# Performance work log

Measured on AMD Instinct MI355X. Metric: run time of the kernel, lower is better.

## Reference

```python
import jax, jax.numpy as jnp
import numpy as np
import math

VOCAB = 32000
HIDDEN = 256
N_HEADS = 8
HEAD_DIM = 32
MAX_LEN = 2048


def _pos_encoding(max_len, d_model, dtype=jnp.float32):
    # Matches PositionalEncoding buffer (even d_model).
    pos = jnp.arange(max_len, dtype=dtype)[:, None]                       # [L,1]
    div = jnp.exp(jnp.arange(0, d_model, 2, dtype=dtype) * (-(math.log(10000.0) / d_model)))
    ang = pos * div                                                        # [L, d/2]
    pe = jnp.zeros((max_len, d_model), dtype=dtype)
    pe = pe.at[:, 0::2].set(jnp.sin(ang))
    pe = pe.at[:, 1::2].set(jnp.cos(ang))
    return pe


def setup_inputs() -> dict:
    key = jax.random.key(0)
    ks = jax.random.split(key, 7)
    B, S = 8, 2047
    s = 0.02
    x = jax.random.randint(ks[0], (B, S), 0, VOCAB + 1, dtype=jnp.int64)
    emb_w = jax.random.normal(ks[1], (VOCAB + 1, HIDDEN), jnp.float32) * s
    wq = jax.random.normal(ks[2], (N_HEADS, HEAD_DIM, HIDDEN), jnp.float32) * s
    wk = jax.random.normal(ks[3], (N_HEADS, HEAD_DIM, HIDDEN), jnp.float32) * s
    wv = jax.random.normal(ks[4], (N_HEADS, HEAD_DIM, HIDDEN), jnp.float32) * s
    wo = jax.random.normal(ks[5], (HIDDEN, N_HEADS * HEAD_DIM), jnp.float32) * s
    wu = jax.random.normal(ks[6], (VOCAB + 1, HIDDEN), jnp.float32) * s
    return {"x": x, "emb_w": emb_w, "wq": wq, "wk": wk, "wv": wv, "wo": wo, "wu": wu}


def reference(x, emb_w, wq, wk, wv, wo, wu):
    B, S = x.shape
    # prepend CLS token (id=2)
    tok = jnp.concatenate([jnp.full((B, 1), 2, dtype=x.dtype), x], axis=1)  # [B, S+1]
    y = emb_w[tok]                                                          # [B, S+1, H]
    y = y + _pos_encoding(S + 1, HIDDEN, y.dtype)
    # batched per-head QKV (nn.Linear: out = in @ W.T)
    q = jnp.einsum('bsh,nkh->bnsk', y, wq)
    k = jnp.einsum('bsh,nkh->bnsk', y, wk)
    v = jnp.einsum('bsh,nkh->bnsk', y, wv)
    scores = jnp.einsum('bnsk,bntk->bnst', q, k) / (HEAD_DIM ** 0.5)        # [B,N,S+1,S+1]
    A = jax.nn.softmax(scores, axis=-1)
    o = jnp.einsum('bnst,bntk->bnsk', A, v)                                 # [B,N,S+1,K]
    o = jnp.transpose(o, (0, 2, 1, 3)).reshape(B, S + 1, N_HEADS * HEAD_DIM)
    att = o @ wo.T + y     # residual inside MultiHeadAttention
    y = att + y            # second residual in MultiHeadTransformerPosEmb.forward
    out = y[:, 0, :] @ wu.T                                                 # [B, VOCAB+1]
    return out
```

## Files before the change

kernel.cpp:

```cpp
#include <hip/hip_runtime.h>
#include <stdint.h>

#define B_   8
#define S_   2047
#define L_   2048
#define H_   256
#define NH_  8
#define HD_  32
#define V_   32001

__device__ __forceinline__ float foldx(float a, int off) {
    return a + __shfl_xor(a, off, 64);
}
__device__ __forceinline__ float sel8(const float a[8], int j) {
    float v = a[0];
    v = (j == 1) ? a[1] : v;
    v = (j == 2) ? a[2] : v;
    v = (j == 3) ? a[3] : v;
    v = (j == 4) ? a[4] : v;
    v = (j == 5) ? a[5] : v;
    v = (j == 6) ? a[6] : v;
    v = (j == 7) ? a[7] : v;
    return v;
}

__global__ __launch_bounds__(256) void k0_prep(const float* __restrict__ emb,
                                               const float* __restrict__ wq,
                                               const float* __restrict__ wk,
                                               float* __restrict__ qk,
                                               float* __restrict__ y0,
                                               int* __restrict__ counters) {
    __shared__ float y0_l[H_];
    __shared__ float q0p[HD_][8];
    __shared__ float q0_l[HD_];
    int n = blockIdx.x, tid = threadIdx.x;
    if (tid == 0) counters[n] = 0;
    float v = emb[2 * H_ + tid] + ((tid & 1) ? 1.0f : 0.0f);
    y0_l[tid] = v;
    if (n == 0) y0[tid] = v;
    __syncthreads();
    {
        int k = tid >> 3, part = tid & 7;
        const float* w = wq + (n * HD_ + k) * H_ + part * 32;
        const float* yy = y0_l + part * 32;
        float acc = 0.f;
#pragma unroll
        for (int j = 0; j < 32; ++j) acc += w[j] * yy[j];
        q0p[k][part] = acc;
    }
    __syncthreads();
    if (tid < HD_) {
        float s = 0.f;
#pragma unroll
        for (int j = 0; j < 8; ++j) s += q0p[tid][j];
        q0_l[tid] = s;
    }
    __syncthreads();
    float acc = 0.f;
    for (int k = 0; k < HD_; ++k)
        acc += q0_l[k] * wk[(n * HD_ + k) * H_ + tid];
    qk[n * H_ + tid] = acc * 0.17677669529663687f;
}

__global__ __launch_bounds__(256, 1) void k13_attn(const int* __restrict__ x,
                                                   const float* __restrict__ emb,
                                                   const float* __restrict__ qkw,
                                                   const float* __restrict__ wv,
                                                   const float* __restrict__ wo,
                                                   const float* __restrict__ y0g,
                                                   float* __restrict__ op_partial,
                                                   float* __restrict__ esum_blk,
                                                   float* __restrict__ z,
                                                   int* __restrict__ counters) {
    int bid = blockIdx.x;
    int b = bid >> 5, c = bid & 31;
    int tid = threadIdx.x, lane = tid & 63, w = tid >> 6;
    int t0 = c * 64 + w * 16;

    __shared__ float4 p_l4[64][2];
    __shared__ __align__(16) float red[4][NH_ * H_];
    __shared__ float es_l[4][NH_];
    __shared__ int is_last;
    __shared__ float inv_l[NH_];
    __shared__ float o_l[H_];

    float4 qr[NH_];
#pragma unroll
    for (int n = 0; n < NH_; ++n)
        qr[n] = *(const float4*)(qkw + n * H_ + lane * 4);

    const float cdiv = 0.07195578414202881f;
    float div0 = expf(-(float)(lane * 2) * cdiv);
    float div1 = expf(-(float)(lane * 2 + 1) * cdiv);
    float s0, c0, s1, c1, sd0, cd0, sd1, cd1;
    {
        float a0 = (float)t0 * div0, a1 = (float)t0 * div1;
        s0 = sinf(a0); c0 = cosf(a0); s1 = sinf(a1); c1 = cosf(a1);
        sd0 = sinf(div0); cd0 = cosf(div0);
        sd1 = sinf(div1); cd1 = cosf(div1);
    }

    float4 yreg[16];
    float es = 0.f;

#pragma unroll
    for (int i = 0; i < 16; ++i) {
        int t = t0 + i;
        int tok = (t == 0) ? 2 : x[b * S_ + t - 1];
        float4 ev = *(const float4*)(emb + (size_t)tok * H_ + lane * 4);
        float4 y4;
        y4.x = ev.x + s0; y4.y = ev.y + c0; y4.z = ev.z + s1; y4.w = ev.w + c1;
        yreg[i] = y4;
        float ns0 = s0 * cd0 + c0 * sd0; c0 = c0 * cd0 - s0 * sd0; s0 = ns0;
        float ns1 = s1 * cd1 + c1 * sd1; c1 = c1 * cd1 - s1 * sd1; s1 = ns1;

        float a[NH_];
#pragma unroll
        for (int n = 0; n < NH_; ++n)
            a[n] = qr[n].x * y4.x + qr[n].y * y4.y + qr[n].z * y4.z + qr[n].w * y4.w;
        float m4[4];
#pragma unroll
        for (int k = 0; k < 4; ++k) {
            float lo = foldx(a[k], 32), hi = foldx(a[k + 4], 32);
            m4[k] = (lane & 32) ? hi : lo;
        }
        float m2[2];
#pragma unroll
        for (int k = 0; k < 2; ++k) {
            float lo = foldx(m4[k], 16), hi = foldx(m4[k + 2], 16);
            m2[k] = (lane & 16) ? hi : lo;
        }
        float lo = foldx(m2[0], 8), hi = foldx(m2[1], 8);
        float m1 = (lane & 8) ? hi : lo;
        m1 = foldx(m1, 4); m1 = foldx(m1, 2); m1 = foldx(m1, 1);
        float e = __expf(m1);
        es += e;
        if ((lane & 7) == 0)
            ((float*)&p_l4[w * 16 + i][0])[lane >> 3] = e;
    }
    if ((lane & 7) == 0) es_l[w][lane >> 3] = es;

    float4 acc4[NH_];
#pragma unroll
    for (int n = 0; n < NH_; ++n) acc4[n] = make_float4(0.f, 0.f, 0.f, 0.f);
#pragma unroll
    for (int i = 0; i < 16; ++i) {
        float4 pA = p_l4[w * 16 + i][0];
        float4 pB = p_l4[w * 16 + i][1];
        float p[NH_] = {pA.x, pA.y, pA.z, pA.w, pB.x, pB.y, pB.z, pB.w};
        float4 y4 = yreg[i];
#pragma unroll
        for (int n = 0; n < NH_; ++n) {
            acc4[n].x += p[n] * y4.x;
            acc4[n].y += p[n] * y4.y;
            acc4[n].z += p[n] * y4.z;
            acc4[n].w += p[n] * y4.w;
        }
    }
#pragma unroll
    for (int n = 0; n < NH_; ++n)
        *(float4*)&red[w][n * H_ + lane * 4] = acc4[n];
    __syncthreads();
#pragma unroll
    for (int g = 0; g < 2; ++g) {
        int idx = tid * 8 + g * 4;
        float4 r0 = *(const float4*)&red[0][idx];
        float4 r1 = *(const float4*)&red[1][idx];
        float4 r2 = *(const float4*)&red[2][idx];
        float4 r3 = *(const float4*)&red[3][idx];
        float4 s;
        s.x = r0.x + r1.x + r2.x + r3.x;
        s.y = r0.y + r1.y + r2.y + r3.y;
        s.z = r0.z + r1.z + r2.z + r3.z;
        s.w = r0.w + r1.w + r2.w + r3.w;
        *(float4*)&red[0][idx] = s;
    }
    if (tid < NH_)
        esum_blk[bid * NH_ + tid] = es_l[0][tid] + es_l[1][tid] + es_l[2][tid] + es_l[3][tid];
    __syncthreads();
    {
        int n = tid >> 5;
        const float* wrow = wv + (size_t)tid * H_;
        const float* ps = &red[0][n * H_];
        float acc = 0.f;
#pragma unroll 16
        for (int h4 = 0; h4 < H_ / 4; ++h4) {
            float4 wv4 = *(const float4*)(wrow + h4 * 4);
            float4 p4 = *(const float4*)(ps + h4 * 4);
            acc += wv4.x * p4.x + wv4.y * p4.y + wv4.z * p4.z + wv4.w * p4.w;
        }
        op_partial[bid * H_ + tid] = acc;
    }

    __threadfence();
    __syncthreads();
    if (tid == 0) is_last = (atomicAdd(&counters[b], 1) == 31);
    __syncthreads();
    if (!is_last) return;
    __threadfence();

    if (tid < NH_) {
        float s = 0.f;
#pragma unroll
        for (int cc = 0; cc < 32; ++cc) s += esum_blk[(b * 32 + cc) * NH_ + tid];
        inv_l[tid] = 1.0f / s;
    }
    __syncthreads();
    {
        float s = 0.f;
#pragma unroll
        for (int cc = 0; cc < 32; ++cc) s += op_partial[(b * 32 + cc) * H_ + tid];
        o_l[tid] = s * inv_l[tid >> 5];
    }
    __syncthreads();
    {
        const float* wrow = wo + (size_t)tid * H_;
        float s = 0.f;
#pragma unroll 16
        for (int j4 = 0; j4 < H_ / 4; ++j4) {
            float4 w4 = *(const float4*)(wrow + j4 * 4);
            s += w4.x * o_l[j4 * 4] + w4.y * o_l[j4 * 4 + 1]
               + w4.z * o_l[j4 * 4 + 2] + w4.w * o_l[j4 * 4 + 3];
        }
        z[b * H_ + tid] = s + 2.0f * y0g[tid];
    }
}

__global__ __launch_bounds__(256) void k5_out(const float* __restrict__ z,
                                              const float* __restrict__ wu,
                                              float* __restrict__ out) {
    int tid = threadIdx.x, lane = tid & 63, w = tid >> 6;
    int m = lane & 15;
    int g = lane >> 4;
    int hb = m * 16;
    float zr[B_][16];
#pragma unroll
    for (int b = 0; b < B_; ++b)
#pragma unroll
        for (int jj = 0; jj < 4; ++jj)
            *(float4*)&zr[b][jj * 4] = *(const float4*)(z + b * H_ + hb + jj * 4);

    __shared__ float o_l[B_ * 65];
    int base = blockIdx.x * 64;
#pragma unroll
    for (int pass = 0; pass < 4; ++pass) {
        int rl = w * 16 + pass * 4 + g;
        int v = base + rl;
        int vc = (v < V_) ? v : (V_ - 1);
        const float* wr = wu + (size_t)vc * H_ + hb;
        float4 w0 = *(const float4*)(wr);
        float4 w1 = *(const float4*)(wr + 4);
        float4 w2 = *(const float4*)(wr + 8);
        float4 w3 = *(const float4*)(wr + 12);
        float acc[B_];
#pragma unroll
        for (int b = 0; b < B_; ++b) {
            acc[b] = zr[b][0] * w0.x + zr[b][1] * w0.y + zr[b][2] * w0.z + zr[b][3] * w0.w
                   + zr[b][4] * w1.x + zr[b][5] * w1.y + zr[b][6] * w1.z + zr[b][7] * w1.w
                   + zr[b][8] * w2.x + zr[b][9] * w2.y + zr[b][10] * w2.z + zr[b][11] * w2.w
                   + zr[b][12] * w3.x + zr[b][13] * w3.y + zr[b][14] * w3.z + zr[b][15] * w3.w;
        }
#pragma unroll
        for (int off = 1; off <= 8; off <<= 1) {
#pragma unroll
            for (int b = 0; b < B_; ++b) acc[b] += __shfl_xor(acc[b], off, 64);
        }
        if (m < B_) o_l[m * 65 + rl] = sel8(acc, m);
    }
    __syncthreads();
    for (int i = tid; i < B_ * 64; i += 256) {
        int b = i >> 6, vl = i & 63, v = base + vl;
        if (v < V_) out[b * V_ + v] = o_l[b * 65 + vl];
    }
}

extern "C" void kernel_launch(void* const* d_in, const int* in_sizes, int n_in,
                              void* d_out, int out_size, void* d_ws, size_t ws_size,
                              hipStream_t stream) {
    const int*   x   = (const int*)d_in[0];
    const float* emb = (const float*)d_in[1];
    const float* wq  = (const float*)d_in[2];
    const float* wk  = (const float*)d_in[3];
    const float* wv  = (const float*)d_in[4];
    const float* wo  = (const float*)d_in[5];
    const float* wu  = (const float*)d_in[6];
    float*       out = (float*)d_out;

    float* qk       = (float*)d_ws;
    float* y0       = qk + NH_ * H_;
    float* z        = y0 + H_;
    float* esum_blk = z + B_ * H_;
    float* op_part  = esum_blk + 256 * NH_;
    int*   counters = (int*)(op_part + 256 * H_);

    k0_prep <<<8,   256, 0, stream>>>(emb, wq, wk, qk, y0, counters);
    k13_attn<<<256, 256, 0, stream>>>(x, emb, qk, wv, wo, y0, op_part, esum_blk, z, counters);
    k5_out  <<<(V_ + 63) / 64, 256, 0, stream>>>(z, wu, out);
}
```

Measured before the change: 181.2 us.

## Split fused attention kernel into score and weighted-sum kernels with bf16 y cache

Replaces the single 256-block attention kernel with two kernels. The first uses 4096 blocks, one wave per token, to compute scores and write exp values plus a bf16 copy of y to workspace. The second uses 512 blocks to accumulate weighted y per head and does the last-block reduction, and it now applies Wv after averaging rather than per chunk. This is meant to raise parallelism and cut register pressure, at the cost of an extra launch, global round-trips through the workspace, and bf16 rounding of y in the weighted sum.

After: 236.0 us. +30.3%, slower.

```diff
diff --git a/kernel.cpp b/kernel.cpp
--- a/kernel.cpp
+++ b/kernel.cpp
@@ -8,7 +8,18 @@
 #define NH_  8
 #define HD_  32
 #define V_   32001
-
+#define NCH_ 64
+#define TCH_ 32
+
+__device__ __forceinline__ float b2f(unsigned short u) {
+    union { uint32_t i; float f; } c; c.i = ((uint32_t)u) << 16; return c.f;
+}
+__device__ __forceinline__ unsigned short f2b(float f) {
+    union { float f; uint32_t i; } c; c.f = f;
+    uint32_t x = c.i;
+    uint32_t r = (x + 0x7fffu + ((x >> 16) & 1u)) >> 16;
+    return (unsigned short)r;
+}
 __device__ __forceinline__ float foldx(float a, int off) {
     return a + __shfl_xor(a, off, 64);
 }
@@ -62,155 +73,142 @@
     qk[n * H_ + tid] = acc * 0.17677669529663687f;
 }
 
-__global__ __launch_bounds__(256, 1) void k13_attn(const int* __restrict__ x,
-                                                   const float* __restrict__ emb,
-                                                   const float* __restrict__ qkw,
-                                                   const float* __restrict__ wv,
-                                                   const float* __restrict__ wo,
-                                                   const float* __restrict__ y0g,
-                                                   float* __restrict__ op_partial,
-                                                   float* __restrict__ esum_blk,
-                                                   float* __restrict__ z,
-                                                   int* __restrict__ counters) {
+__global__ __launch_bounds__(256) void k1_scores(const int* __restrict__ x,
+                                                 const float* __restrict__ emb,
+                                                 const float* __restrict__ qkw,
+                                                 unsigned short* __restrict__ ycache,
+                                                 float* __restrict__ Et) {
+    int tid  = threadIdx.x;
+    int lane = tid & 63;
+    int gid  = blockIdx.x * 4 + (tid >> 6);
+    int b = gid >> 11, t = gid & (L_ - 1);
+    int h0 = lane * 4;
+
+    float4 qr[NH_];
+#pragma unroll
+    for (int n = 0; n < NH_; ++n)
+        qr[n] = *(const float4*)(qkw + n * H_ + h0);
+
+    const float cdiv = 0.07195578414202881f;
+    float div0 = __expf(-(float)(lane * 2) * cdiv);
+    float div1 = __expf(-(float)(lane * 2 + 1) * cdiv);
+    float a0 = (float)t * div0, a1 = (float)t * div1;
+    float s0 = __sinf(a0), c0 = __cosf(a0);
+    float s1 = __sinf(a1), c1 = __cosf(a1);
+
+    int tok = (t == 0) ? 2 : x[b * S_ + t - 1];
+    float4 ev = *(const float4*)(emb + (size_t)tok * H_ + h0);
+    float4 y4;
+    y4.x = ev.x + s0; y4.y = ev.y + c0; y4.z = ev.z + s1; y4.w = ev.w + c1;
+    ushort4 st;
+    st.x = f2b(y4.x); st.y = f2b(y4.y); st.z = f2b(y4.z); st.w = f2b(y4.w);
+    *(ushort4*)(ycache + ((size_t)gid << 8) + h0) = st;
+
+    float a[NH_];
+#pragma unroll
+    for (int n = 0; n < NH_; ++n)
+        a[n] = qr[n].x * y4.x + qr[n].y * y4.y + qr[n].z * y4.z + qr[n].w * y4.w;
+    float m4[4];
+#pragma unroll
+    for (int k = 0; k < 4; ++k) {
+        float lo = foldx(a[k], 32), hi = foldx(a[k + 4], 32);
+        m4[k] = (lane & 32) ? hi : lo;
+    }
+    float m2[2];
+#pragma unroll
+    for (int k = 0; k < 2; ++k) {
+        float lo = foldx(m4[k], 16), hi = foldx(m4[k + 2], 16);
+        m2[k] = (lane & 16) ? hi : lo;
+    }
+    float lo = foldx(m2[0], 8), hi = foldx(m2[1], 8);
+    float m1 = (lane & 8) ? hi : lo;
+    m1 = foldx(m1, 4); m1 = foldx(m1, 2); m1 = foldx(m1, 1);
+    float e = __expf(m1);
+    if ((lane & 7) == 0)
+        Et[(size_t)gid * NH_ + (lane >> 3)] = e;
+}
+
+__global__ __launch_bounds__(256) void k3_ybar(const float* __restrict__ Et,
+                                               const unsigned short* __restrict__ ycache,
+                                               const float* __restrict__ wv,
+                                               const float* __restrict__ wo,
+                                               const float* __restrict__ y0g,
+                                               float* __restrict__ psum,
+                                               float* __restrict__ esum_blk,
+                                               float* __restrict__ z,
+                                               int* __restrict__ counters) {
     int bid = blockIdx.x;
-    int b = bid >> 5, c = bid & 31;
-    int tid = threadIdx.x, lane = tid & 63, w = tid >> 6;
-    int t0 = c * 64 + w * 16;
-
-    __shared__ float4 p_l4[64][2];
-    __shared__ __align__(16) float red[4][NH_ * H_];
-    __shared__ float es_l[4][NH_];
+    int b = bid >> 6, c = bid & 63;
+    int t0 = c * TCH_;
+    int tid = threadIdx.x;
+
+    __shared__ float e_l[TCH_ * NH_];
     __shared__ int is_last;
     __shared__ float inv_l[NH_];
+    __shared__ float ybar_l[NH_ * 260];
     __shared__ float o_l[H_];
 
-    float4 qr[NH_];
+    e_l[tid] = Et[(size_t)(b * L_ + t0) * NH_ + tid];
+    __syncthreads();
+    if (tid < NH_) {
+        float s = 0.f;
+#pragma unroll
+        for (int tt = 0; tt < TCH_; ++tt) s += e_l[tt * NH_ + tid];
+        esum_blk[bid * NH_ + tid] = s;
+    }
+
+    float acc[NH_] = {};
+    const unsigned short* yb = ycache + ((size_t)(b * L_ + t0) << 8) + tid;
+#pragma unroll
+    for (int tt = 0; tt < TCH_; ++tt) {
+        float yv = b2f(yb[(size_t)tt << 8]);
+        float4 eA = *(const float4*)&e_l[tt * NH_];
+        float4 eB = *(const float4*)&e_l[tt * NH_ + 4];
+        acc[0] += eA.x * yv; acc[1] += eA.y * yv;
+        acc[2] += eA.z * yv; acc[3] += eA.w * yv;
+        acc[4] += eB.x * yv; acc[5] += eB.y * yv;
+        acc[6] += eB.z * yv; acc[7] += eB.w * yv;
+    }
 #pragma unroll
     for (int n = 0; n < NH_; ++n)
-        qr[n] = *(const float4*)(qkw + n * H_ + lane * 4);
-
-    const float cdiv = 0.07195578414202881f;
-    float div0 = expf(-(float)(lane * 2) * cdiv);
-    float div1 = expf(-(float)(lane * 2 + 1) * cdiv);
-    float s0, c0, s1, c1, sd0, cd0, sd1, cd1;
-    {
-        float a0 = (float)t0 * div0, a1 = (float)t0 * div1;
-        s0 = sinf(a0); c0 = cosf(a0); s1 = sinf(a1); c1 = cosf(a1);
-        sd0 = sinf(div0); cd0 = cosf(div0);
-        sd1 = sinf(div1); cd1 = cosf(div1);
-    }
-
-    float4 yreg[16];
-    float es = 0.f;
-
-#pragma unroll
-    for (int i = 0; i < 16; ++i) {
-        int t = t0 + i;
-        int tok = (t == 0) ? 2 : x[b * S_ + t - 1];
-        float4 ev = *(const float4*)(emb + (size_t)tok * H_ + lane * 4);
-        float4 y4;
-        y4.x = ev.x + s0; y4.y = ev.y + c0; y4.z = ev.z + s1; y4.w = ev.w + c1;
-        yreg[i] = y4;
-        float ns0 = s0 * cd0 + c0 * sd0; c0 = c0 * cd0 - s0 * sd0; s0 = ns0;
-        float ns1 = s1 * cd1 + c1 * sd1; c1 = c1 * cd1 - s1 * sd1; s1 = ns1;
-
-        float a[NH_];
-#pragma unroll
-        for (int n = 0; n < NH_; ++n)
-            a[n] = qr[n].x * y4.x + qr[n].y * y4.y + qr[n].z * y4.z + qr[n].w * y4.w;
-        float m4[4];
-#pragma unroll
-        for (int k = 0; k < 4; ++k) {
-            float lo = foldx(a[k], 32), hi = foldx(a[k + 4], 32);
-            m4[k] = (lane & 32) ? hi : lo;
-        }
-        float m2[2];
-#pragma unroll
-        for (int k = 0; k < 2; ++k) {
-            float lo = foldx(m4[k], 16), hi = foldx(m4[k + 2], 16);
-            m2[k] = (lane & 16) ? hi : lo;
-        }
-        float lo = foldx(m2[0], 8), hi = foldx(m2[1], 8);
-        float m1 = (lane & 8) ? hi : lo;
-        m1 = foldx(m1, 4); m1 = foldx(m1, 2); m1 = foldx(m1, 1);
-        float e = __expf(m1);
-        es += e;
-        if ((lane & 7) == 0)
-            ((float*)&p_l4[w * 16 + i][0])[lane >> 3] = e;
-    }
-    if ((lane & 7) == 0) es_l[w][lane >> 3] = es;
-
-    float4 acc4[NH_];
-#pragma unroll
-    for (int n = 0; n < NH_; ++n) acc4[n] = make_float4(0.f, 0.f, 0.f, 0.f);
-#pragma unroll
-    for (int i = 0; i < 16; ++i) {
-        float4 pA = p_l4[w * 16 + i][0];
-        float4 pB = p_l4[w * 16 + i][1];
-        float p[NH_] = {pA.x, pA.y, pA.z, pA.w, pB.x, pB.y, pB.z, pB.w};
-        float4 y4 = yreg[i];
-#pragma unroll
-        for (int n = 0; n < NH_; ++n) {
-            acc4[n].x += p[n] * y4.x;
-            acc4[n].y += p[n] * y4.y;
-            acc4[n].z += p[n] * y4.z;
-            acc4[n].w += p[n] * y4.w;
-        }
-    }
-#pragma unroll
-    for (int n = 0; n < NH_; ++n)
-        *(float4*)&red[w][n * H_ + lane * 4] = acc4[n];
-    __syncthreads();
-#pragma unroll
-    for (int g = 0; g < 2; ++g) {
-        int idx = tid * 8 + g * 4;
-        float4 r0 = *(const float4*)&red[0][idx];
-        float4 r1 = *(const float4*)&red[1][idx];
-        float4 r2 = *(const float4*)&red[2][idx];
-        float4 r3 = *(const float4*)&red[3][idx];
-        float4 s;
-        s.x = r0.x + r1.x + r2.x + r3.x;
-        s.y = r0.y + r1.y + r2.y + r3.y;
-        s.z = r0.z + r1.z + r2.z + r3.z;
-        s.w = r0.w + r1.w + r2.w + r3.w;
-        *(float4*)&red[0][idx] = s;
-    }
-    if (tid < NH_)
-        esum_blk[bid * NH_ + tid] = es_l[0][tid] + es_l[1][tid] + es_l[2][tid] + es_l[3][tid];
+        psum[((size_t)bid * NH_ + n) * H_ + tid] = acc[n];
+
+    __threadfence();
+    __syncthreads();
+    if (tid == 0) is_last = (atomicAdd(&counters[b], 1) == NCH_ - 1);
+    __syncthreads();
+    if (!is_last) return;
+    __threadfence();
+
+    if (tid < NH_) {
+        float s = 0.f;
+#pragma unroll 8
+        for (int cc = 0; cc < NCH_; ++cc)
+            s += esum_blk[(b * NCH_ + cc) * NH_ + tid];
+        inv_l[tid] = 1.0f / s;
+    }
+    __syncthreads();
+#pragma unroll
+    for (int n = 0; n < NH_; ++n) {
+        const float* pp = psum + ((size_t)(b * NCH_) * NH_ + n) * H_ + tid;
+        float s = 0.f;
+#pragma unroll 8
+        for (int cc = 0; cc < NCH_; ++cc) s += pp[(size_t)cc * NH_ * H_];
+        ybar_l[n * 260 + tid] = s * inv_l[n];
+    }
     __syncthreads();
     {
         int n = tid >> 5;
         const float* wrow = wv + (size_t)tid * H_;
-        const float* ps = &red[0][n * H_];
-        float acc = 0.f;
+        const float* yy = ybar_l + n * 260;
+        float s = 0.f;
 #pragma unroll 16
         for (int h4 = 0; h4 < H_ / 4; ++h4) {
-            float4 wv4 = *(const float4*)(wrow + h4 * 4);
-            float4 p4 = *(const float4*)(ps + h4 * 4);
-            acc += wv4.x * p4.x + wv4.y * p4.y + wv4.z * p4.z + wv4.w * p4.w;
+            float4 w4 = *(const float4*)(wrow + h4 * 4);
+            float4 p4 = *(const float4*)(yy + h4 * 4);
+            s += w4.x * p4.x + w4.y * p4.y + w4.z * p4.z + w4.w * p4.w;
         }
-        op_partial[bid * H_ + tid] = acc;
-    }
-
-    __threadfence();
-    __syncthreads();
-    if (tid == 0) is_last = (atomicAdd(&counters[b], 1) == 31);
-    __syncthreads();
-    if (!is_last) return;
-    __threadfence();
-
-    if (tid < NH_) {
-        float s = 0.f;
-#pragma unroll
-        for (int cc = 0; cc < 32; ++cc) s += esum_blk[(b * 32 + cc) * NH_ + tid];
-        inv_l[tid] = 1.0f / s;
-    }
-    __syncthreads();
-    {
-        float s = 0.f;
-#pragma unroll
-        for (int cc = 0; cc < 32; ++cc) s += op_partial[(b * 32 + cc) * H_ + tid];
-        o_l[tid] = s * inv_l[tid >> 5];
+        o_l[tid] = s;
     }
     __syncthreads();
     {
@@ -290,10 +288,13 @@
     float* y0       = qk + NH_ * H_;
     float* z        = y0 + H_;
     float* esum_blk = z + B_ * H_;
-    float* op_part  = esum_blk + 256 * NH_;
-    int*   counters = (int*)(op_part + 256 * H_);
-
-    k0_prep <<<8,   256, 0, stream>>>(emb, wq, wk, qk, y0, counters);
-    k13_attn<<<256, 256, 0, stream>>>(x, emb, qk, wv, wo, y0, op_part, esum_blk, z, counters);
-    k5_out  <<<(V_ + 63) / 64, 256, 0, stream>>>(z, wu, out);
-}
+    float* psum     = esum_blk + 512 * NH_;
+    float* Et       = psum + (size_t)512 * NH_ * H_;
+    int*   counters = (int*)(Et + (size_t)B_ * L_ * NH_);
+    unsigned short* ycache = (unsigned short*)(counters + 16);
+
+    k0_prep  <<<8,    256, 0, stream>>>(emb, wq, wk, qk, y0, counters);
+    k1_scores<<<4096, 256, 0, stream>>>(x, emb, qk, ycache, Et);
+    k3_ybar  <<<512,  256, 0, stream>>>(Et, ycache, wv, wo, y0, psum, esum_blk, z, counters);
+    k5_out   <<<(V_ + 63) / 64, 256, 0, stream>>>(z, wu, out);
+}
```
